# Performance work log

Measured on AMD Instinct MI355X. Metric: run time of the kernel, lower is better.

## Reference

```python
import jax, jax.numpy as jnp
import numpy as np

N_HEADS = 16
HEAD_SIZE = 64
EMBED = 1024
BLOCK = 2048
B, T = 2, 2048


def setup_inputs() -> dict:
    key = jax.random.key(0)
    ks = jax.random.split(key, 6)
    scale = 0.02
    inputs = jax.random.normal(ks[0], (B, T, EMBED), dtype=jnp.float32)
    # per-head projection weights, stacked: [H, E, D]
    Wk = jax.random.normal(ks[1], (N_HEADS, EMBED, HEAD_SIZE), dtype=jnp.float32) * scale
    Wq = jax.random.normal(ks[2], (N_HEADS, EMBED, HEAD_SIZE), dtype=jnp.float32) * scale
    Wv = jax.random.normal(ks[3], (N_HEADS, EMBED, HEAD_SIZE), dtype=jnp.float32) * scale
    Wo = jax.random.normal(ks[4], (EMBED, EMBED), dtype=jnp.float32) * scale
    bo = jax.random.normal(ks[5], (EMBED,), dtype=jnp.float32) * scale
    return {"inputs": inputs, "Wk": Wk, "Wq": Wq, "Wv": Wv, "Wo": Wo, "bo": bo}


def reference(inputs, Wk, Wq, Wv, Wo, bo):
    # per-head projections: [B,H,T,D]
    k = jnp.einsum("bte,hed->bhtd", inputs, Wk)
    q = jnp.einsum("bte,hed->bhtd", inputs, Wq)
    v = jnp.einsum("bte,hed->bhtd", inputs, Wv)
    # NOTE: original computes wei = K @ Q^T (faithful reproduction)
    wei = jnp.einsum("bhtd,bhsd->bhts", k, q) * (HEAD_SIZE ** -0.5)
    causal = jnp.tril(jnp.ones((T, T), dtype=bool))  # tril==0 masked
    wei = jnp.where(causal, wei, -jnp.inf)
    wei = jax.nn.softmax(wei, axis=-1)
    out = jnp.einsum("bhts,bhsd->bhtd", wei, v)
    # concat heads along feature dim: [B,T,H*D]
    z = out.transpose(0, 2, 1, 3).reshape(B, T, N_HEADS * HEAD_SIZE)
    z = z @ Wo.T + bo  # match torch Linear(x) = x @ W^T + b
    return z
```

## Files before the change

### kernel.cpp

```cpp
#include <hip/hip_runtime.h>
#include <cstdint>
#include <cstddef>

typedef __bf16 bf8_t __attribute__((ext_vector_type(8)));
typedef float  f4_t  __attribute__((ext_vector_type(4)));

static __device__ __forceinline__ f4_t mfma16(bf8_t a, bf8_t b, f4_t c) {
    return __builtin_amdgcn_mfma_f32_16x16x32_bf16(a, b, c, 0, 0, 0);
}

#if defined(__has_builtin) && __has_builtin(__builtin_amdgcn_exp2f)
#define EXP2F(x) __builtin_amdgcn_exp2f(x)
#else
#define EXP2F(x) exp2f(x)
#endif

static __device__ __forceinline__ void async_ld16(const __bf16* g, __bf16* l) {
    __builtin_amdgcn_global_load_lds(
        (const __attribute__((address_space(1))) void*)(uintptr_t)g,
        (__attribute__((address_space(3))) void*)(uintptr_t)l, 16, 0, 0);
}


__global__ void __launch_bounds__(256) prep_all(const float* __restrict__ X,
                                                const float* __restrict__ Wo,
                                                const float* __restrict__ Wq,
                                                const float* __restrict__ Wk,
                                                const float* __restrict__ Wv,
                                                __bf16* __restrict__ Xbf,
                                                __bf16* __restrict__ Wobf,
                                                __bf16* __restrict__ Wqt,
                                                __bf16* __restrict__ Wkt,
                                                __bf16* __restrict__ Wvt) {
    __shared__ float tile[64][65];
    int bx = (int)blockIdx.x;
    if (bx < 2560) {
        const float* src; __bf16* dst; size_t base;
        if (bx < 2048) { src = X;  dst = Xbf;  base = (size_t)bx * 2048; }
        else           { src = Wo; dst = Wobf; base = (size_t)(bx - 2048) * 2048; }
        size_t i = base + (size_t)threadIdx.x * 8;
        float4 a = *(const float4*)(src + i);
        float4 b = *(const float4*)(src + i + 4);
        bf8_t o;
        o[0] = (__bf16)a.x; o[1] = (__bf16)a.y; o[2] = (__bf16)a.z; o[3] = (__bf16)a.w;
        o[4] = (__bf16)b.x; o[5] = (__bf16)b.y; o[6] = (__bf16)b.z; o[7] = (__bf16)b.w;
        *(bf8_t*)(dst + i) = o;
        return;
    }
    int wt = bx - 2560;
    int which = wt >> 8, inner = wt & 255;
    const float* W; __bf16* Wt;
    if (which == 0)      { W = Wq; Wt = Wqt; }
    else if (which == 1) { W = Wk; Wt = Wkt; }
    else                 { W = Wv; Wt = Wvt; }
    int h = inner >> 4, eb = inner & 15;
    int tx = threadIdx.x;
    int e = tx >> 2, dg = (tx & 3) * 16;
    const float* src = W + ((size_t)h * 1024 + eb * 64 + e) * 64 + dg;
#pragma unroll
    for (int i = 0; i < 4; ++i) {
        float4 v = *(const float4*)(src + i * 4);
        tile[dg + i * 4 + 0][e] = v.x;
        tile[dg + i * 4 + 1][e] = v.y;
        tile[dg + i * 4 + 2][e] = v.z;
        tile[dg + i * 4 + 3][e] = v.w;
    }
    __syncthreads();
    int d = tx >> 2, eg = (tx & 3) * 16;
    __bf16* dst = Wt + (size_t)(h * 64 + d) * 1024 + eb * 64 + eg;
    bf8_t o0, o1;
#pragma unroll
    for (int i = 0; i < 8; ++i) o0[i] = (__bf16)tile[d][eg + i];
#pragma unroll
    for (int i = 0; i < 8; ++i) o1[i] = (__bf16)tile[d][eg + 8 + i];
    *(bf8_t*)dst       = o0;
    *(bf8_t*)(dst + 8) = o1;
}

static __device__ __forceinline__ void gemm_tile128(const __bf16* __restrict__ A,
                                                    const __bf16* __restrict__ Bt,
                                                    __bf16* As, __bf16* Bs,
                                                    int m0, int n0, f4_t acc[4][4]) {
    const int tid  = threadIdx.x;
    const int lane = tid & 63;
    const int wv   = tid >> 6;
    const int lrow = lane >> 3;
    const int lsc  = lane & 7;
    const int quad = lane >> 4;
    const int l15  = lane & 15;
    const int wm = (wv & 1) * 64;
    const int wn = (wv >> 1) * 64;
    f4_t zero = {0.f, 0.f, 0.f, 0.f};
#pragma unroll
    for (int mi = 0; mi < 4; ++mi)
#pragma unroll
        for (int ni = 0; ni < 4; ++ni) acc[mi][ni] = zero;

    for (int kb = 0; kb < 16; ++kb) {
#pragma unroll
        for (int j = 0; j < 4; ++j) {
            int row = wv * 32 + j * 8 + lrow;
            int lc  = lsc ^ (row & 7);
            async_ld16(A + (size_t)(m0 + row) * 1024 + kb * 64 + lc * 8,
                       As + (wv * 32 + j * 8) * 64);
            async_ld16(Bt + (size_t)(n0 + row) * 1024 + kb * 64 + lc * 8,
                       Bs + (wv * 32 + j * 8) * 64);
        }
        __syncthreads();
#pragma unroll
        for (int ks = 0; ks < 2; ++ks) {
            bf8_t af[4], bfr[4];
#pragma unroll
            for (int mi = 0; mi < 4; ++mi) {
                int row = wm + mi * 16 + l15;
                int ch  = (ks * 4 + quad) ^ (row & 7);
                af[mi] = *(const bf8_t*)(As + row * 64 + ch * 8);
            }
#pragma unroll
            for (int ni = 0; ni < 4; ++ni) {
                int row = wn + ni * 16 + l15;
                int ch  = (ks * 4 + quad) ^ (row & 7);
                bfr[ni] = *(const bf8_t*)(Bs + row * 64 + ch * 8);
            }
#pragma unroll
            for (int mi = 0; mi < 4; ++mi)
#pragma unroll
                for (int ni = 0; ni < 4; ++ni)
                    acc[mi][ni] = mfma16(af[mi], bfr[ni], acc[mi][ni]);
        }
        __syncthreads();
    }
}

__global__ void __launch_bounds__(256, 3) gemm_proj(const __bf16* __restrict__ Xbf,
                                                    const __bf16* __restrict__ Wqt,
                                                    const __bf16* __restrict__ Wkt,
                                                    const __bf16* __restrict__ Wvt,
                                                    __bf16* __restrict__ Qb,
                                                    __bf16* __restrict__ Kb,
                                                    __bf16* __restrict__ Vt) {
    __shared__ __bf16 smem[17408];
    __bf16* As = smem;
    __bf16* Bs = smem + 8192;
    int which = blockIdx.y;
    const __bf16* Bt = which == 0 ? Wqt : (which == 1 ? Wkt : Wvt);
    int m0 = ((int)blockIdx.x >> 3) * 128;
    int n0 = ((int)blockIdx.x & 7) * 128;
    f4_t acc[4][4];
    gemm_tile128(Xbf, Bt, As, Bs, m0, n0, acc);
    const int lane = threadIdx.x & 63, wv = threadIdx.x >> 6;
    const int quad = lane >> 4, l15 = lane & 15;
    const int wm = (wv & 1) * 64, wn = (wv >> 1) * 64;
    const int STR = 136;
    if (which < 2) {
        __bf16* C = which ? Kb : Qb;
        const float scl = which ? 0.18033688f : 1.0f;
#pragma unroll
        for (int mi = 0; mi < 4; ++mi)
#pragma unroll
            for (int ni = 0; ni < 4; ++ni)
#pragma unroll
                for (int r = 0; r < 4; ++r) {
                    int ml = wm + mi * 16 + quad * 4 + r;
                    int nl = wn + ni * 16 + l15;
                    smem[ml * STR + nl] = (__bf16)(acc[mi][ni][r] * scl);
                }
        __syncthreads();
        int row = (int)threadIdx.x >> 1;
        int seg = (int)threadIdx.x & 1;
        int m = m0 + row;
        int b = m >> 11, t = m & 2047;
        int h = (n0 >> 6) + seg;
        __bf16* dst = C + ((size_t)(b * 16 + h) * 2048 + t) * 64;
        const __bf16* srcl = smem + row * STR + seg * 64;
#pragma unroll
        for (int k = 0; k < 8; ++k)
            *(bf8_t*)(dst + k * 8) = *(const bf8_t*)(srcl + k * 8);
    } else {
#pragma unroll
        for (int mi = 0; mi < 4; ++mi)
#pragma unroll
            for (int ni = 0; ni < 4; ++ni)
#pragma unroll
                for (int r = 0; r < 4; ++r) {
                    int ml = wm + mi * 16 + quad * 4 + r;
                    int nl = wn + ni * 16 + l15;
                    smem[nl * STR + ml] = (__bf16)acc[mi][ni][r];
                }
        __syncthreads();
        int b = m0 >> 11, tg0 = m0 & 2047;
        int nl = (int)threadIdx.x >> 1;
        int tc = ((int)threadIdx.x & 1) * 64;
        int n = n0 + nl, h = n >> 6, d = n & 63;
        __bf16* dst = Vt + ((size_t)(b * 16 + h) * 64 + d) * 2048 + tg0 + tc;
        const __bf16* srcl = smem + nl * STR + tc;
#pragma unroll
        for (int k = 0; k < 8; ++k)
            *(bf8_t*)(dst + k * 8) = *(const bf8_t*)(srcl + k * 8);
    }
}

static __device__ __forceinline__ void gemm_tile(const __bf16* __restrict__ A,
                                                 const __bf16* __restrict__ Bt,
                                                 __bf16* As, __bf16* Bs,
                                                 int m0, int n0, f4_t acc[4][2]) {
    const int tid  = threadIdx.x;
    const int lane = tid & 63;
    const int wv   = tid >> 6;
    const int lrow = lane >> 3;
    const int lsc  = lane & 7;
    const int quad = lane >> 4;
    const int l15  = lane & 15;
    const int wm = (wv & 1) * 64;
    const int wn = (wv >> 1) * 32;
    f4_t zero = {0.f, 0.f, 0.f, 0.f};
#pragma unroll
    for (int mi = 0; mi < 4; ++mi)
#pragma unroll
        for (int ni = 0; ni < 2; ++ni) acc[mi][ni] = zero;

    for (int kb = 0; kb < 16; ++kb) {
#pragma unroll
        for (int j = 0; j < 4; ++j) {
            int row = wv * 32 + j * 8 + lrow;
            int lc  = lsc ^ (row & 7);
            async_ld16(A + (size_t)(m0 + row) * 1024 + kb * 64 + lc * 8,
                       As + (wv * 32 + j * 8) * 64);
        }
#pragma unroll
        for (int j = 0; j < 2; ++j) {
            int row = wv * 16 + j * 8 + lrow;
            int lc  = lsc ^ (row & 7);
            async_ld16(Bt + (size_t)(n0 + row) * 1024 + kb * 64 + lc * 8,
                       Bs + (wv * 16 + j * 8) * 64);
        }
        __syncthreads();
#pragma unroll
        for (int ks = 0; ks < 2; ++ks) {
            bf8_t af[4], bfr[2];
#pragma unroll
            for (int mi = 0; mi < 4; ++mi) {
                int row = wm + mi * 16 + l15;
                int ch  = (ks * 4 + quad) ^ (row & 7);
                af[mi] = *(const bf8_t*)(As + row * 64 + ch * 8);
            }
#pragma unroll
            for (int ni = 0; ni < 2; ++ni) {
                int row = wn + ni * 16 + l15;
                int ch  = (ks * 4 + quad) ^ (row & 7);
                bfr[ni] = *(const bf8_t*)(Bs + row * 64 + ch * 8);
            }
#pragma unroll
            for (int mi = 0; mi < 4; ++mi)
#pragma unroll
                for (int ni = 0; ni < 2; ++ni)
                    acc[mi][ni] = mfma16(af[mi], bfr[ni], acc[mi][ni]);
        }
        __syncthreads();
    }
}

__global__ void __launch_bounds__(256) gemm_out(const __bf16* __restrict__ Ob,
                                                const __bf16* __restrict__ Wobf,
                                                const float* __restrict__ bo,
                                                float* __restrict__ out) {
    __shared__ __bf16 smem[128 * 64 + 64 * 64];
    __bf16* As = smem;
    __bf16* Bs = smem + 128 * 64;
    int m0 = ((int)blockIdx.x >> 4) * 128;
    int n0 = ((int)blockIdx.x & 15) * 64;
    f4_t acc[4][2];
    gemm_tile(Ob, Wobf, As, Bs, m0, n0, acc);
    const int lane = threadIdx.x & 63, wv = threadIdx.x >> 6;
    const int quad = lane >> 4, l15 = lane & 15;
    const int wm = (wv & 1) * 64, wn = (wv >> 1) * 32;
#pragma unroll
    for (int mi = 0; mi < 4; ++mi)
#pragma unroll
        for (int ni = 0; ni < 2; ++ni)
#pragma unroll
            for (int r = 0; r < 4; ++r) {
                int m = m0 + wm + mi * 16 + quad * 4 + r;
                int n = n0 + wn + ni * 16 + l15;
                out[(size_t)m * 1024 + n] = acc[mi][ni][r] + bo[n];
            }
}

__global__ void __launch_bounds__(256, 3) attn(const __bf16* __restrict__ Kb,
                                               const __bf16* __restrict__ Qb,
                                               const __bf16* __restrict__ Vt,
                                               __bf16* __restrict__ Ob,
                                               int* __restrict__ ctrs) {
    __shared__ __bf16 Qs[2][64 * 64];
    __shared__ __bf16 Vs[2][64 * 64];
    __shared__ __bf16 Ps[4][16 * 72];
    __shared__ int item_lds;
    const int tid = threadIdx.x, lane = tid & 63, wv = tid >> 6;
    const int quad = lane >> 4, l15 = lane & 15;
    const int lrow8 = lane >> 3, lchunk = lane & 7;
    int xcc;
    asm volatile("s_getreg_b32 %0, hwreg(HW_REG_XCC_ID)" : "=s"(xcc));
    xcc &= 7;
    int* ctr = ctrs + xcc * 16;
    __bf16* Psw = &Ps[wv][0];
    f4_t zero = {0.f, 0.f, 0.f, 0.f};

    for (;;) {
        if (tid == 0) item_lds = atomicAdd(ctr, 1);
        __syncthreads();
        const int q = item_lds;
        if (q >= 128) break;
        const int tt = 31 - (q >> 2);
        const int bh = xcc * 4 + (q & 3);
        const int b = bh >> 4, h = bh & 15;
        const int t0 = tt * 64;
        const int tw = t0 + wv * 16;
        const __bf16* Kp = Kb + (size_t)bh * 2048 * 64;
        const __bf16* Qp = Qb + (size_t)bh * 2048 * 64;
        const __bf16* Vp = Vt + (size_t)bh * 64 * 2048;

        bf8_t kfrag[2];
#pragma unroll
        for (int ks = 0; ks < 2; ++ks)
            kfrag[ks] = *(const bf8_t*)(Kp + (size_t)(tw + l15) * 64 + ks * 32 + quad * 8);

        f4_t oacc[4];
#pragma unroll
        for (int ni = 0; ni < 4; ++ni) oacc[ni] = zero;
        float lsum[4] = {0.f, 0.f, 0.f, 0.f};

        auto stage = [&](int buf, int s0) {
#pragma unroll
            for (int j = 0; j < 2; ++j) {
                int row = wv * 8 + j * 32 + lrow8;
                int cg  = lchunk ^ (row & 7);
                async_ld16(Qp + (size_t)(s0 + row) * 64 + cg * 8,
                           &Qs[buf][(wv * 8 + j * 32) * 64]);
                async_ld16(Vp + (size_t)row * 2048 + s0 + cg * 8,
                           &Vs[buf][(wv * 8 + j * 32) * 64]);
            }
        };

        const int nsb = tt + 1;
        stage(0, 0);
        for (int sb = 0; sb < nsb; ++sb) {
            const int cur = sb & 1;
            const int s0 = sb * 64;
            const bool masked = (sb == nsb - 1);
            __syncthreads();
            if (sb + 1 < nsb) stage(1 ^ cur, s0 + 64);
            const __bf16* Qc = &Qs[cur][0];
            const __bf16* Vc = &Vs[cur][0];
            f4_t sacc[4] = {zero, zero, zero, zero};
#pragma unroll
            for (int ks = 0; ks < 2; ++ks) {
                bf8_t qf[4];
#pragma unroll
                for (int st = 0; st < 4; ++st) {
                    int row = st * 16 + l15;
                    int ch  = (ks * 4 + quad) ^ (row & 7);
                    qf[st] = *(const bf8_t*)(Qc + row * 64 + ch * 8);
                }
#pragma unroll
                for (int st = 0; st < 4; ++st)
                    sacc[st] = mfma16(kfrag[ks], qf[st], sacc[st]);
            }
#pragma unroll
            for (int st = 0; st < 4; ++st)
#pragma unroll
                for (int r = 0; r < 4; ++r) {
                    float e = EXP2F(sacc[st][r]);
                    if (masked && (s0 + st * 16 + l15 > tw + quad * 4 + r)) e = 0.0f;
                    lsum[r] += e;
                    Psw[(quad * 4 + r) * 72 + st * 16 + l15] = (__bf16)e;
                }
            asm volatile("s_waitcnt lgkmcnt(0)" ::: "memory");
            bf8_t pf[2];
#pragma unroll
            for (int ks = 0; ks < 2; ++ks)
                pf[ks] = *(const bf8_t*)(Psw + l15 * 72 + ks * 32 + quad * 8);
#pragma unroll
            for (int ks = 0; ks < 2; ++ks) {
                bf8_t vf[4];
#pragma unroll
                for (int ni = 0; ni < 4; ++ni) {
                    int row = ni * 16 + l15;
                    int ch  = (ks * 4 + quad) ^ (row & 7);
                    vf[ni] = *(const bf8_t*)(Vc + row * 64 + ch * 8);
                }
#pragma unroll
                for (int ni = 0; ni < 4; ++ni)
                    oacc[ni] = mfma16(pf[ks], vf[ni], oacc[ni]);
            }
        }

#pragma unroll
        for (int r = 0; r < 4; ++r) {
            float l = lsum[r];
            l += __shfl_xor(l, 1);
            l += __shfl_xor(l, 2);
            l += __shfl_xor(l, 4);
            l += __shfl_xor(l, 8);
            float inv = 1.0f / l;
            int t = tw + quad * 4 + r;
#pragma unroll
            for (int ni = 0; ni < 4; ++ni)
                Ob[((size_t)(b * 2048 + t) * 16 + h) * 64 + ni * 16 + l15] =
                    (__bf16)(oacc[ni][r] * inv);
        }
    }
}

extern "C" void kernel_launch(void* const* d_in, const int* in_sizes, int n_in,
                              void* d_out, int out_size, void* d_ws, size_t ws_size,
                              hipStream_t stream) {
    const float* X  = (const float*)d_in[0];
    const float* Wk = (const float*)d_in[1];
    const float* Wq = (const float*)d_in[2];
    const float* Wv = (const float*)d_in[3];
    const float* Wo = (const float*)d_in[4];
    const float* bo = (const float*)d_in[5];
    float* out = (float*)d_out;

    __bf16* ws   = (__bf16*)d_ws;
    __bf16* Xbf  = ws;
    __bf16* Wqt  = ws + 4194304;
    __bf16* Wkt  = ws + 5242880;
    __bf16* Wvt  = ws + 6291456;
    __bf16* Wobf = ws + 7340032;
    __bf16* Qb   = ws + 8388608;
    __bf16* Kb   = ws + 12582912;
    __bf16* Vt   = ws + 16777216;
    __bf16* Ob   = ws + 20971520;
    int* ctrs = (int*)d_ws;

    prep_all<<<3328, 256, 0, stream>>>(X, Wo, Wq, Wk, Wv, Xbf, Wobf, Wqt, Wkt, Wvt);
    gemm_proj<<<dim3(256, 3), 256, 0, stream>>>(Xbf, Wqt, Wkt, Wvt, Qb, Kb, Vt);
    hipMemsetAsync(ctrs, 0, 512, stream);
    attn<<<768, 256, 0, stream>>>(Kb, Qb, Vt, Ob, ctrs);
    gemm_out<<<512, 256, 0, stream>>>(Ob, Wobf, bo, out);
}
```

Measured before the change: 171.9 us.

## Widen attention key tiles to 128 and use 128x128 output GEMM tiles

The attention loop now stages 128 Q rows and 128 V columns per iteration with a 16-way swizzle for the wider V tile. The score-to-PV step runs in two halves so the per-wave P buffer stays the same size. This halves the number of barrier and staging steps. The output projection switches from 128x64 to 128x128 tiles (via gemm_tile128, assumed defined in the unseen part) and hoists the bias load. The larger LDS footprint lowers attention occupancy to 2 blocks per CU, and the causal diagonal tile now wastes more work when 128-wide tiles meet 64-row query tiles.

```diff
diff --git a/kernel.cpp b/kernel.cpp
--- a/kernel.cpp
+++ b/kernel.cpp
@@ -200,104 +200,45 @@
     }
 }
 
-static __device__ __forceinline__ void gemm_tile(const __bf16* __restrict__ A,
-                                                 const __bf16* __restrict__ Bt,
-                                                 __bf16* As, __bf16* Bs,
-                                                 int m0, int n0, f4_t acc[4][2]) {
-    const int tid  = threadIdx.x;
-    const int lane = tid & 63;
-    const int wv   = tid >> 6;
-    const int lrow = lane >> 3;
-    const int lsc  = lane & 7;
-    const int quad = lane >> 4;
-    const int l15  = lane & 15;
-    const int wm = (wv & 1) * 64;
-    const int wn = (wv >> 1) * 32;
-    f4_t zero = {0.f, 0.f, 0.f, 0.f};
-#pragma unroll
-    for (int mi = 0; mi < 4; ++mi)
-#pragma unroll
-        for (int ni = 0; ni < 2; ++ni) acc[mi][ni] = zero;
-
-    for (int kb = 0; kb < 16; ++kb) {
-#pragma unroll
-        for (int j = 0; j < 4; ++j) {
-            int row = wv * 32 + j * 8 + lrow;
-            int lc  = lsc ^ (row & 7);
-            async_ld16(A + (size_t)(m0 + row) * 1024 + kb * 64 + lc * 8,
-                       As + (wv * 32 + j * 8) * 64);
-        }
-#pragma unroll
-        for (int j = 0; j < 2; ++j) {
-            int row = wv * 16 + j * 8 + lrow;
-            int lc  = lsc ^ (row & 7);
-            async_ld16(Bt + (size_t)(n0 + row) * 1024 + kb * 64 + lc * 8,
-                       Bs + (wv * 16 + j * 8) * 64);
-        }
-        __syncthreads();
-#pragma unroll
-        for (int ks = 0; ks < 2; ++ks) {
-            bf8_t af[4], bfr[2];
-#pragma unroll
-            for (int mi = 0; mi < 4; ++mi) {
-                int row = wm + mi * 16 + l15;
-                int ch  = (ks * 4 + quad) ^ (row & 7);
-                af[mi] = *(const bf8_t*)(As + row * 64 + ch * 8);
-            }
-#pragma unroll
-            for (int ni = 0; ni < 2; ++ni) {
-                int row = wn + ni * 16 + l15;
-                int ch  = (ks * 4 + quad) ^ (row & 7);
-                bfr[ni] = *(const bf8_t*)(Bs + row * 64 + ch * 8);
-            }
-#pragma unroll
-            for (int mi = 0; mi < 4; ++mi)
-#pragma unroll
-                for (int ni = 0; ni < 2; ++ni)
-                    acc[mi][ni] = mfma16(af[mi], bfr[ni], acc[mi][ni]);
-        }
-        __syncthreads();
-    }
-}
-
 __global__ void __launch_bounds__(256) gemm_out(const __bf16* __restrict__ Ob,
                                                 const __bf16* __restrict__ Wobf,
                                                 const float* __restrict__ bo,
                                                 float* __restrict__ out) {
-    __shared__ __bf16 smem[128 * 64 + 64 * 64];
+    __shared__ __bf16 smem[16384];
     __bf16* As = smem;
-    __bf16* Bs = smem + 128 * 64;
-    int m0 = ((int)blockIdx.x >> 4) * 128;
-    int n0 = ((int)blockIdx.x & 15) * 64;
-    f4_t acc[4][2];
-    gemm_tile(Ob, Wobf, As, Bs, m0, n0, acc);
+    __bf16* Bs = smem + 8192;
+    int m0 = ((int)blockIdx.x >> 3) * 128;
+    int n0 = ((int)blockIdx.x & 7) * 128;
+    f4_t acc[4][4];
+    gemm_tile128(Ob, Wobf, As, Bs, m0, n0, acc);
     const int lane = threadIdx.x & 63, wv = threadIdx.x >> 6;
     const int quad = lane >> 4, l15 = lane & 15;
-    const int wm = (wv & 1) * 64, wn = (wv >> 1) * 32;
+    const int wm = (wv & 1) * 64, wn = (wv >> 1) * 64;
 #pragma unroll
     for (int mi = 0; mi < 4; ++mi)
 #pragma unroll
-        for (int ni = 0; ni < 2; ++ni)
+        for (int ni = 0; ni < 4; ++ni) {
+            float bias = bo[n0 + wn + ni * 16 + l15];
 #pragma unroll
             for (int r = 0; r < 4; ++r) {
                 int m = m0 + wm + mi * 16 + quad * 4 + r;
                 int n = n0 + wn + ni * 16 + l15;
-                out[(size_t)m * 1024 + n] = acc[mi][ni][r] + bo[n];
-            }
-}
-
-__global__ void __launch_bounds__(256, 3) attn(const __bf16* __restrict__ Kb,
+                out[(size_t)m * 1024 + n] = acc[mi][ni][r] + bias;
+            }
+        }
+}
+
+__global__ void __launch_bounds__(256, 2) attn(const __bf16* __restrict__ Kb,
                                                const __bf16* __restrict__ Qb,
                                                const __bf16* __restrict__ Vt,
                                                __bf16* __restrict__ Ob,
                                                int* __restrict__ ctrs) {
-    __shared__ __bf16 Qs[2][64 * 64];
-    __shared__ __bf16 Vs[2][64 * 64];
+    __shared__ __bf16 Qs[2][128 * 64];
+    __shared__ __bf16 Vs[2][64 * 128];
     __shared__ __bf16 Ps[4][16 * 72];
     __shared__ int item_lds;
     const int tid = threadIdx.x, lane = tid & 63, wv = tid >> 6;
     const int quad = lane >> 4, l15 = lane & 15;
-    const int lrow8 = lane >> 3, lchunk = lane & 7;
     int xcc;
     asm volatile("s_getreg_b32 %0, hwreg(HW_REG_XCC_ID)" : "=s"(xcc));
     xcc &= 7;
@@ -331,66 +272,78 @@
 
         auto stage = [&](int buf, int s0) {
 #pragma unroll
-            for (int j = 0; j < 2; ++j) {
-                int row = wv * 8 + j * 32 + lrow8;
-                int cg  = lchunk ^ (row & 7);
-                async_ld16(Qp + (size_t)(s0 + row) * 64 + cg * 8,
-                           &Qs[buf][(wv * 8 + j * 32) * 64]);
-                async_ld16(Vp + (size_t)row * 2048 + s0 + cg * 8,
-                           &Vs[buf][(wv * 8 + j * 32) * 64]);
+            for (int j = 0; j < 4; ++j) {
+                int qbase = wv * 32 + j * 8;
+                int qrow = qbase + (lane >> 3);
+                int qch  = (lane & 7) ^ (qrow & 7);
+                async_ld16(Qp + (size_t)(s0 + qrow) * 64 + qch * 8,
+                           &Qs[buf][qbase * 64]);
+                int vbase = wv * 16 + j * 4;
+                int vrow = vbase + (lane >> 4);
+                int vch  = (lane & 15) ^ (vrow & 15);
+                async_ld16(Vp + (size_t)vrow * 2048 + s0 + vch * 8,
+                           &Vs[buf][vbase * 128]);
             }
         };
 
-        const int nsb = tt + 1;
+        const int nsb = (tt >> 1) + 1;
         stage(0, 0);
         for (int sb = 0; sb < nsb; ++sb) {
             const int cur = sb & 1;
-            const int s0 = sb * 64;
+            const int s0 = sb * 128;
             const bool masked = (sb == nsb - 1);
             __syncthreads();
-            if (sb + 1 < nsb) stage(1 ^ cur, s0 + 64);
+            if (sb + 1 < nsb) stage(1 ^ cur, s0 + 128);
             const __bf16* Qc = &Qs[cur][0];
             const __bf16* Vc = &Vs[cur][0];
-            f4_t sacc[4] = {zero, zero, zero, zero};
+            f4_t sacc[8];
+#pragma unroll
+            for (int st = 0; st < 8; ++st) sacc[st] = zero;
 #pragma unroll
             for (int ks = 0; ks < 2; ++ks) {
-                bf8_t qf[4];
-#pragma unroll
-                for (int st = 0; st < 4; ++st) {
+                bf8_t qf[8];
+#pragma unroll
+                for (int st = 0; st < 8; ++st) {
                     int row = st * 16 + l15;
                     int ch  = (ks * 4 + quad) ^ (row & 7);
                     qf[st] = *(const bf8_t*)(Qc + row * 64 + ch * 8);
                 }
 #pragma unroll
+                for (int st = 0; st < 8; ++st)
+                    sacc[st] = mfma16(kfrag[ks], qf[st], sacc[st]);
+            }
+#pragma unroll
+            for (int hf = 0; hf < 2; ++hf) {
+#pragma unroll
                 for (int st = 0; st < 4; ++st)
-                    sacc[st] = mfma16(kfrag[ks], qf[st], sacc[st]);
-            }
-#pragma unroll
-            for (int st = 0; st < 4; ++st)
-#pragma unroll
-                for (int r = 0; r < 4; ++r) {
-                    float e = EXP2F(sacc[st][r]);
-                    if (masked && (s0 + st * 16 + l15 > tw + quad * 4 + r)) e = 0.0f;
-                    lsum[r] += e;
-                    Psw[(quad * 4 + r) * 72 + st * 16 + l15] = (__bf16)e;
+#pragma unroll
+                    for (int r = 0; r < 4; ++r) {
+                        int stg = hf * 4 + st;
+                        float e = EXP2F(sacc[stg][r]);
+                        if (masked && (s0 + stg * 16 + l15 > tw + quad * 4 + r)) e = 0.0f;
+                        lsum[r] += e;
+                        Psw[(quad * 4 + r) * 72 + st * 16 + l15] = (__bf16)e;
+                    }
+                asm volatile("s_waitcnt lgkmcnt(0)" ::: "memory");
+                bf8_t pf[2];
+#pragma unroll
+                for (int k2 = 0; k2 < 2; ++k2)
+                    pf[k2] = *(const bf8_t*)(Psw + l15 * 72 + k2 * 32 + quad * 8);
+#pragma unroll
+                for (int k2 = 0; k2 < 2; ++k2) {
+                    int ksg = hf * 2 + k2;
+                    bf8_t vf[4];
+#pragma unroll
+                    for (int ni = 0; ni < 4; ++ni) {
+                        int row = ni * 16 + l15;
+                        int ch  = (ksg * 4 + quad) ^ (row & 15);
+                        vf[ni] = *(const bf8_t*)(Vc + row * 128 + ch * 8);
+                    }
+#pragma unroll
+                    for (int ni = 0; ni < 4; ++ni)
+                        oacc[ni] = mfma16(pf[k2], vf[ni], oacc[ni]);
                 }
-            asm volatile("s_waitcnt lgkmcnt(0)" ::: "memory");
-            bf8_t pf[2];
-#pragma unroll
-            for (int ks = 0; ks < 2; ++ks)
-                pf[ks] = *(const bf8_t*)(Psw + l15 * 72 + ks * 32 + quad * 8);
-#pragma unroll
-            for (int ks = 0; ks < 2; ++ks) {
-                bf8_t vf[4];
-#pragma unroll
-                for (int ni = 0; ni < 4; ++ni) {
-                    int row = ni * 16 + l15;
-                    int ch  = (ks * 4 + quad) ^ (row & 7);
-                    vf[ni] = *(const bf8_t*)(Vc + row * 64 + ch * 8);
-                }
-#pragma unroll
-                for (int ni = 0; ni < 4; ++ni)
-                    oacc[ni] = mfma16(pf[ks], vf[ni], oacc[ni]);
+                asm volatile("s_waitcnt lgkmcnt(0)" ::: "memory");
             }
         }
 
@@ -437,6 +390,6 @@
     prep_all<<<3328, 256, 0, stream>>>(X, Wo, Wq, Wk, Wv, Xbf, Wobf, Wqt, Wkt, Wvt);
     gemm_proj<<<dim3(256, 3), 256, 0, stream>>>(Xbf, Wqt, Wkt, Wvt, Qb, Kb, Vt);
     hipMemsetAsync(ctrs, 0, 512, stream);
-    attn<<<768, 256, 0, stream>>>(Kb, Qb, Vt, Ob, ctrs);
-    gemm_out<<<512, 256, 0, stream>>>(Ob, Wobf, bo, out);
-}
+    attn<<<512, 256, 0, stream>>>(Kb, Qb, Vt, Ob, ctrs);
+    gemm_out<<<256, 256, 0, stream>>>(Ob, Wobf, bo, out);
+}
```

After: 182.7 us. 6.3% more time.

## Use 128-wide single-buffered key tiles in attention with mask-specialized body

Applied to the files above, without the earlier changes.

The attention loop now stages 128 keys per iteration into one buffer instead of double-buffering 64-key tiles. This halves the number of block barriers and loop iterations, and a template-like flag lets the compiler drop the mask test on unmasked tiles. In exchange, the prefetch overlap is lost: each tile is loaded and then waited on before compute, with two barriers per iteration. The output GEMM also hoists the bias load out of the inner row loop.

```diff
diff --git a/kernel.cpp b/kernel.cpp
--- a/kernel.cpp
+++ b/kernel.cpp
@@ -277,13 +277,15 @@
 #pragma unroll
     for (int mi = 0; mi < 4; ++mi)
 #pragma unroll
-        for (int ni = 0; ni < 2; ++ni)
+        for (int ni = 0; ni < 2; ++ni) {
+            float bias = bo[n0 + wn + ni * 16 + l15];
 #pragma unroll
             for (int r = 0; r < 4; ++r) {
                 int m = m0 + wm + mi * 16 + quad * 4 + r;
                 int n = n0 + wn + ni * 16 + l15;
-                out[(size_t)m * 1024 + n] = acc[mi][ni][r] + bo[n];
-            }
+                out[(size_t)m * 1024 + n] = acc[mi][ni][r] + bias;
+            }
+        }
 }
 
 __global__ void __launch_bounds__(256, 3) attn(const __bf16* __restrict__ Kb,
@@ -291,13 +293,12 @@
                                                const __bf16* __restrict__ Vt,
                                                __bf16* __restrict__ Ob,
                                                int* __restrict__ ctrs) {
-    __shared__ __bf16 Qs[2][64 * 64];
-    __shared__ __bf16 Vs[2][64 * 64];
+    __shared__ __bf16 Qs[128 * 64];
+    __shared__ __bf16 Vs[64 * 128];
     __shared__ __bf16 Ps[4][16 * 72];
     __shared__ int item_lds;
     const int tid = threadIdx.x, lane = tid & 63, wv = tid >> 6;
     const int quad = lane >> 4, l15 = lane & 15;
-    const int lrow8 = lane >> 3, lchunk = lane & 7;
     int xcc;
     asm volatile("s_getreg_b32 %0, hwreg(HW_REG_XCC_ID)" : "=s"(xcc));
     xcc &= 7;
@@ -329,69 +330,81 @@
         for (int ni = 0; ni < 4; ++ni) oacc[ni] = zero;
         float lsum[4] = {0.f, 0.f, 0.f, 0.f};
 
-        auto stage = [&](int buf, int s0) {
-#pragma unroll
-            for (int j = 0; j < 2; ++j) {
-                int row = wv * 8 + j * 32 + lrow8;
-                int cg  = lchunk ^ (row & 7);
-                async_ld16(Qp + (size_t)(s0 + row) * 64 + cg * 8,
-                           &Qs[buf][(wv * 8 + j * 32) * 64]);
-                async_ld16(Vp + (size_t)row * 2048 + s0 + cg * 8,
-                           &Vs[buf][(wv * 8 + j * 32) * 64]);
+        auto stage = [&](int s0) {
+#pragma unroll
+            for (int j = 0; j < 4; ++j) {
+                int qbase = wv * 32 + j * 8;
+                int qrow = qbase + (lane >> 3);
+                int qch  = (lane & 7) ^ (qrow & 7);
+                async_ld16(Qp + (size_t)(s0 + qrow) * 64 + qch * 8,
+                           &Qs[qbase * 64]);
+                int vbase = wv * 16 + j * 4;
+                int vrow = vbase + (lane >> 4);
+                int vch  = (lane & 15) ^ (vrow & 15);
+                async_ld16(Vp + (size_t)vrow * 2048 + s0 + vch * 8,
+                           &Vs[vbase * 128]);
             }
         };
 
-        const int nsb = tt + 1;
-        stage(0, 0);
-        for (int sb = 0; sb < nsb; ++sb) {
-            const int cur = sb & 1;
-            const int s0 = sb * 64;
-            const bool masked = (sb == nsb - 1);
-            __syncthreads();
-            if (sb + 1 < nsb) stage(1 ^ cur, s0 + 64);
-            const __bf16* Qc = &Qs[cur][0];
-            const __bf16* Vc = &Vs[cur][0];
-            f4_t sacc[4] = {zero, zero, zero, zero};
+        auto body = [&](int s0, bool MASK) {
+            f4_t sacc[8];
+#pragma unroll
+            for (int st = 0; st < 8; ++st) sacc[st] = zero;
 #pragma unroll
             for (int ks = 0; ks < 2; ++ks) {
-                bf8_t qf[4];
-#pragma unroll
-                for (int st = 0; st < 4; ++st) {
+                bf8_t qf[8];
+#pragma unroll
+                for (int st = 0; st < 8; ++st) {
                     int row = st * 16 + l15;
                     int ch  = (ks * 4 + quad) ^ (row & 7);
-                    qf[st] = *(const bf8_t*)(Qc + row * 64 + ch * 8);
+                    qf[st] = *(const bf8_t*)(Qs + row * 64 + ch * 8);
                 }
 #pragma unroll
+                for (int st = 0; st < 8; ++st)
+                    sacc[st] = mfma16(kfrag[ks], qf[st], sacc[st]);
+            }
+#pragma unroll
+            for (int hf = 0; hf < 2; ++hf) {
+#pragma unroll
                 for (int st = 0; st < 4; ++st)
-                    sacc[st] = mfma16(kfrag[ks], qf[st], sacc[st]);
-            }
-#pragma unroll
-            for (int st = 0; st < 4; ++st)
-#pragma unroll
-                for (int r = 0; r < 4; ++r) {
-                    float e = EXP2F(sacc[st][r]);
-                    if (masked && (s0 + st * 16 + l15 > tw + quad * 4 + r)) e = 0.0f;
-                    lsum[r] += e;
-                    Psw[(quad * 4 + r) * 72 + st * 16 + l15] = (__bf16)e;
+#pragma unroll
+                    for (int r = 0; r < 4; ++r) {
+                        int stg = hf * 4 + st;
+                        float e = EXP2F(sacc[stg][r]);
+                        if (MASK && (s0 + stg * 16 + l15 > tw + quad * 4 + r)) e = 0.0f;
+                        lsum[r] += e;
+                        Psw[(quad * 4 + r) * 72 + st * 16 + l15] = (__bf16)e;
+                    }
+                asm volatile("s_waitcnt lgkmcnt(0)" ::: "memory");
+                bf8_t pf[2];
+#pragma unroll
+                for (int k2 = 0; k2 < 2; ++k2)
+                    pf[k2] = *(const bf8_t*)(Psw + l15 * 72 + k2 * 32 + quad * 8);
+#pragma unroll
+                for (int k2 = 0; k2 < 2; ++k2) {
+                    int ksg = hf * 2 + k2;
+                    bf8_t vf[4];
+#pragma unroll
+                    for (int ni = 0; ni < 4; ++ni) {
+                        int row = ni * 16 + l15;
+                        int ch  = (ksg * 4 + quad) ^ (row & 15);
+                        vf[ni] = *(const bf8_t*)(Vs + row * 128 + ch * 8);
+                    }
+#pragma unroll
+                    for (int ni = 0; ni < 4; ++ni)
+                        oacc[ni] = mfma16(pf[k2], vf[ni], oacc[ni]);
                 }
-            asm volatile("s_waitcnt lgkmcnt(0)" ::: "memory");
-            bf8_t pf[2];
-#pragma unroll
-            for (int ks = 0; ks < 2; ++ks)
-                pf[ks] = *(const bf8_t*)(Psw + l15 * 72 + ks * 32 + quad * 8);
-#pragma unroll
-            for (int ks = 0; ks < 2; ++ks) {
-                bf8_t vf[4];
-#pragma unroll
-                for (int ni = 0; ni < 4; ++ni) {
-                    int row = ni * 16 + l15;
-                    int ch  = (ks * 4 + quad) ^ (row & 7);
-                    vf[ni] = *(const bf8_t*)(Vc + row * 64 + ch * 8);
-                }
-#pragma unroll
-                for (int ni = 0; ni < 4; ++ni)
-                    oacc[ni] = mfma16(pf[ks], vf[ni], oacc[ni]);
-            }
+                asm volatile("s_waitcnt lgkmcnt(0)" ::: "memory");
+            }
+        };
+
+        const int nsb = (tt >> 1) + 1;
+        for (int sb = 0; sb < nsb; ++sb) {
+            const int s0 = sb * 128;
+            stage(s0);
+            __syncthreads();
+            if (sb == nsb - 1) body(s0, true); else body(s0, false);
+            __syncthreads();
         }
 
 #pragma unroll
```

New measurement: 201.4 us. +17.2%, slower.
